# Performance work log

Measured on AMD Instinct MI355X. Metric: run time of the kernel, lower is better.

## Reference

```python
import jax, jax.numpy as jnp
import numpy as np

TEMPERATURE = 0.07
EPS = 1e-07


def setup_inputs() -> dict:
    key = jax.random.key(0)
    kf, kl = jax.random.split(key)
    bsz, n_views, d = 4096, 2, 256
    feats = jax.random.normal(kf, (bsz, n_views, d), dtype=jnp.float32)
    # L2-normalize per view, as in standard SupCon pipelines
    feats = feats / jnp.linalg.norm(feats, axis=-1, keepdims=True)
    labels = jax.random.randint(kl, (bsz,), 0, 3, dtype=jnp.int64 if jax.config.jax_enable_x64 else jnp.int32)
    return {"features": feats, "labels": labels}


def reference(features, labels):
    bsz, n_views, d = features.shape
    n = bsz * n_views
    # torch.cat(torch.unbind(features, dim=1), dim=0): views stacked along batch
    contrast_feature = jnp.transpose(features, (1, 0, 2)).reshape(n, d)
    anchor_feature = contrast_feature  # contrast_mode == 'all'

    # label-equality mask with the module's 1e-7 offset, tiled over views
    mask_small = (labels[:, None] == labels[None, :]).astype(jnp.float32) + EPS
    mask = jnp.tile(mask_small, (n_views, n_views))  # [n, n]

    logits_mask = 1.0 - jnp.eye(n, dtype=jnp.float32)  # zero out self-contrast
    mask_pos = mask * logits_mask
    mask_neg = (1.0 - mask) * logits_mask

    similarity = jnp.exp(jnp.matmul(anchor_feature, contrast_feature.T) / TEMPERATURE)
    pos = jnp.sum(similarity * mask_pos, axis=1)
    neg = jnp.sum(similarity * mask_neg, axis=1)
    loss = -jnp.mean(jnp.log(pos / (pos + neg)))
    return loss
```

## Files before the change

kernel.cpp:

```cpp
#include <hip/hip_runtime.h>
#include <cstdint>

#define BSZ   4096
#define NTOT  8192
#define DIM   256
#define BT    128
#define NCB   (NTOT / BT)
#define NBLK  (NCB * (NCB + 1) / 2)
#define INV_T (1.0f/0.07f)

typedef __bf16 bf16x8 __attribute__((ext_vector_type(8)));
typedef float  f32x4  __attribute__((ext_vector_type(4)));

__device__ __forceinline__ unsigned short f2bf(float f) {
  unsigned int u = __float_as_uint(f);
  u = u + 0x7FFFu + ((u >> 16) & 1u);
  return (unsigned short)(u >> 16);
}


__global__ __launch_bounds__(256) void cvt_kernel(const float* __restrict__ F,
                                                  unsigned short* __restrict__ Xf,
                                                  float* __restrict__ gsum,
                                                  int* __restrict__ gcnt) {
  if (blockIdx.x == 0 && threadIdx.x == 0) { *gsum = 0.f; *gcnt = 0; }
  const int v = blockIdx.x * 256 + threadIdx.x;
  const int T = v >> 9;
  const int c = (v >> 4) & 31;
  const int p = v & 15;
  const int r = T * 16 + p;
  const float* src = F + (size_t)(r & (BSZ - 1)) * (2 * DIM) + (r >> 12) * DIM + c * 8;
  const float4 v0 = *(const float4*)src;
  const float4 v1 = *(const float4*)(src + 4);
  ushort4 o0 = make_ushort4(f2bf(v0.x), f2bf(v0.y), f2bf(v0.z), f2bf(v0.w));
  ushort4 o1 = make_ushort4(f2bf(v1.x), f2bf(v1.y), f2bf(v1.z), f2bf(v1.w));
  *(ushort4*)(Xf + (size_t)v * 8)     = o0;
  *(ushort4*)(Xf + (size_t)v * 8 + 4) = o1;
}

__global__ __launch_bounds__(256, 3) void supcon_kernel(
    const unsigned short* __restrict__ Xf, const int* __restrict__ lab,
    float* __restrict__ partTot, float* __restrict__ partEq) {
  __shared__ float sbuf[1024];

  const int tid  = threadIdx.x;
  const int lane = tid & 63;
  const int wave = tid >> 6;
  const int wr   = (wave >> 1) * 64;
  const int wc   = (wave & 1) * 64;
  const int l15  = lane & 15;
  const int quad = lane >> 4;

  const int b = blockIdx.x;
  const int c = (b & 7) * (NBLK / 8) + (b >> 3);
  int i, j;
  if (c < 1792) {
    const int spo = c >> 6;
    const int w   = c & 63;
    int g1 = 0, rem = spo;
    while (rem >= 7 - g1) { rem -= 7 - g1; ++g1; }
    const int g2 = g1 + 1 + rem;
    i = g1 * 8 + (w >> 3);
    j = g2 * 8 + (w & 7);
  } else {
    const int c2 = c - 1792;
    const int g  = c2 / 36;
    int w = c2 - g * 36;
    int a = 0;
    while (w >= 8 - a) { w -= 8 - a; ++a; }
    i = g * 8 + a;
    j = g * 8 + a + w;
  }
  const int RB = i * BT;
  const int CB = j * BT;

  int colIdx[4], colLab[4];
#pragma unroll
  for (int tc = 0; tc < 4; ++tc) {
    colIdx[tc] = CB + wc + tc * 16 + l15;
    colLab[tc] = lab[colIdx[tc] & (BSZ - 1)];
  }
  int rowLab[4][4];
#pragma unroll
  for (int tr = 0; tr < 4; ++tr)
#pragma unroll
    for (int reg = 0; reg < 4; ++reg)
      rowLab[tr][reg] = lab[(RB + wr + tr * 16 + quad * 4 + reg) & (BSZ - 1)];

  const int TA = (RB >> 4) + (wave >> 1) * 4;
  const int TB = (CB >> 4) + (wave & 1) * 4;
  const int lo = quad * 128 + l15 * 8;

  f32x4 acc[4][4] = {};

#pragma unroll
  for (int kb = 0; kb < 8; ++kb) {
    bf16x8 aF[4], bF[4];
    const int ko = kb * 512 + lo;
#pragma unroll
    for (int t = 0; t < 4; ++t) {
      aF[t] = *(const bf16x8*)(Xf + (size_t)(TA + t) * 4096 + ko);
      bF[t] = *(const bf16x8*)(Xf + (size_t)(TB + t) * 4096 + ko);
    }
#pragma unroll
    for (int tr = 0; tr < 4; ++tr)
#pragma unroll
      for (int tc = 0; tc < 4; ++tc)
        acc[tr][tc] = __builtin_amdgcn_mfma_f32_16x16x32_bf16(
            aF[tr], bF[tc], acc[tr][tc], 0, 0, 0);
  }

  if (i == j) {
#pragma unroll
    for (int tr = 0; tr < 4; ++tr)
#pragma unroll
      for (int tc = 0; tc < 4; ++tc)
#pragma unroll
        for (int reg = 0; reg < 4; ++reg) {
          const int row = RB + wr + tr * 16 + quad * 4 + reg;
          float e = __expf(acc[tr][tc][reg] * INV_T);
          acc[tr][tc][reg] = (colIdx[tc] == row) ? 0.f : e;
        }
  } else {
#pragma unroll
    for (int tr = 0; tr < 4; ++tr)
#pragma unroll
      for (int tc = 0; tc < 4; ++tc)
#pragma unroll
        for (int reg = 0; reg < 4; ++reg)
          acc[tr][tc][reg] = __expf(acc[tr][tc][reg] * INV_T);
  }

#pragma unroll
  for (int tr = 0; tr < 4; ++tr) {
#pragma unroll
    for (int reg = 0; reg < 4; ++reg) {
      float tot = 0.f, eqs = 0.f;
#pragma unroll
      for (int tc = 0; tc < 4; ++tc) {
        const float e = acc[tr][tc][reg];
        tot += e;
        if (colLab[tc] == rowLab[tr][reg]) eqs += e;
      }
#pragma unroll
      for (int off = 1; off < 16; off <<= 1) {
        tot += __shfl_xor(tot, off, 64);
        eqs += __shfl_xor(eqs, off, 64);
      }
      if (l15 == 0) {
        const int rl_ = wr + tr * 16 + quad * 4 + reg;
        sbuf[(wave & 1) * 128 + rl_]       = tot;
        sbuf[256 + (wave & 1) * 128 + rl_] = eqs;
      }
    }
  }
  if (i != j) {
#pragma unroll
    for (int tc = 0; tc < 4; ++tc) {
      float tt = 0.f, te = 0.f;
#pragma unroll
      for (int tr = 0; tr < 4; ++tr)
#pragma unroll
        for (int reg = 0; reg < 4; ++reg) {
          const float e = acc[tr][tc][reg];
          tt += e;
          if (rowLab[tr][reg] == colLab[tc]) te += e;
        }
      tt += __shfl_xor(tt, 16, 64);  te += __shfl_xor(te, 16, 64);
      tt += __shfl_xor(tt, 32, 64);  te += __shfl_xor(te, 32, 64);
      if (quad == 0) {
        const int cl_ = wc + tc * 16 + l15;
        sbuf[512 + (wave >> 1) * 128 + cl_] = tt;
        sbuf[768 + (wave >> 1) * 128 + cl_] = te;
      }
    }
  }
  __syncthreads();

  if (tid < 128) {
    partTot[(size_t)j * NTOT + RB + tid] = sbuf[tid] + sbuf[128 + tid];
    partEq [(size_t)j * NTOT + RB + tid] = sbuf[256 + tid] + sbuf[384 + tid];
  } else if (i != j) {
    const int c2 = tid - 128;
    partTot[(size_t)i * NTOT + CB + c2] = sbuf[512 + c2] + sbuf[640 + c2];
    partEq [(size_t)i * NTOT + CB + c2] = sbuf[768 + c2] + sbuf[896 + c2];
  }
}

__global__ __launch_bounds__(128) void reduce_kernel(
    const float* __restrict__ partTot, const float* __restrict__ partEq,
    float* __restrict__ gsum, int* __restrict__ gcnt,
    unsigned int* __restrict__ out) {
  const int r = blockIdx.x * 128 + threadIdx.x;
  float tot = 0.f, eqs = 0.f;
#pragma unroll 8
  for (int cb = 0; cb < NCB; ++cb) {
    tot += partTot[(size_t)cb * NTOT + r];
    eqs += partEq [(size_t)cb * NTOT + r];
  }
  const float term = __logf((eqs + 1e-7f * tot) / tot);
  __shared__ float red[128];
  red[threadIdx.x] = term;
  __syncthreads();
  for (int step = 64; step > 0; step >>= 1) {
    if (threadIdx.x < step) red[threadIdx.x] += red[threadIdx.x + step];
    __syncthreads();
  }
  if (threadIdx.x == 0) {
    atomicAdd(gsum, red[0]);
    __threadfence();
    const int old = atomicAdd(gcnt, 1);
    if (old == (int)gridDim.x - 1) {
      __threadfence();
      const float total = atomicAdd(gsum, 0.0f);
      const float loss = -total / (float)NTOT;
      const unsigned short bb = f2bf(loss);
      out[0] = ((unsigned int)bb << 16) | (unsigned int)bb;
    }
  }
}

extern "C" void kernel_launch(void* const* d_in, const int* in_sizes, int n_in,
                              void* d_out, int out_size, void* d_ws, size_t ws_size,
                              hipStream_t stream) {
  (void)in_sizes; (void)n_in; (void)out_size; (void)ws_size;
  const float* feats = (const float*)d_in[0];
  const int*   labels = (const int*)d_in[1];

  char* ws = (char*)d_ws;
  unsigned short* Xf = (unsigned short*)ws;
  float* partTot = (float*)(ws + (size_t)NTOT * DIM * 2);
  float* partEq  = partTot + (size_t)NCB * NTOT;
  float* gsum    = partEq  + (size_t)NCB * NTOT;
  int*   gcnt    = (int*)(gsum + 1);

  cvt_kernel<<<NTOT * DIM / 8 / 256, 256, 0, stream>>>(feats, Xf, gsum, gcnt);
  supcon_kernel<<<NBLK, 256, 0, stream>>>(Xf, labels, partTot, partEq);
  reduce_kernel<<<NTOT / 128, 128, 0, stream>>>(partTot, partEq, gsum, gcnt,
                                                (unsigned int*)d_out);
}
```

Measured before the change: 106.8 us.

## Switch similarity GEMM from bf16 to scaled fp8 MFMA

Features are now converted to fp8 (scaled by 4 to use more of the dynamic range) instead of bf16, and the Gram matrix uses fp8 MFMA instructions, with the exponent scale adjusted by 1/16 to undo the scaling. The conversion kernel stages rows through LDS to write the new packed fragment layout. This halves operand bytes and uses the higher-throughput fp8 matrix path, at the cost of much lower precision. Logits are divided by 0.07, so fp8 rounding errors are magnified before the exp, which risks loss accuracy.

```diff
diff --git a/kernel.cpp b/kernel.cpp
--- a/kernel.cpp
+++ b/kernel.cpp
@@ -7,10 +7,9 @@
 #define BT    128
 #define NCB   (NTOT / BT)
 #define NBLK  (NCB * (NCB + 1) / 2)
-#define INV_T (1.0f/0.07f)
-
-typedef __bf16 bf16x8 __attribute__((ext_vector_type(8)));
-typedef float  f32x4  __attribute__((ext_vector_type(4)));
+#define INV_T16 (1.0f/(0.07f*16.0f))
+
+typedef float f32x4 __attribute__((ext_vector_type(4)));
 
 __device__ __forceinline__ unsigned short f2bf(float f) {
   unsigned int u = __float_as_uint(f);
@@ -20,26 +19,41 @@
 
 
 __global__ __launch_bounds__(256) void cvt_kernel(const float* __restrict__ F,
-                                                  unsigned short* __restrict__ Xf,
+                                                  unsigned char* __restrict__ Xf,
                                                   float* __restrict__ gsum,
                                                   int* __restrict__ gcnt) {
+  __shared__ unsigned char lds[32 * 264];
   if (blockIdx.x == 0 && threadIdx.x == 0) { *gsum = 0.f; *gcnt = 0; }
-  const int v = blockIdx.x * 256 + threadIdx.x;
-  const int T = v >> 9;
-  const int c = (v >> 4) & 31;
-  const int p = v & 15;
-  const int r = T * 16 + p;
-  const float* src = F + (size_t)(r & (BSZ - 1)) * (2 * DIM) + (r >> 12) * DIM + c * 8;
-  const float4 v0 = *(const float4*)src;
-  const float4 v1 = *(const float4*)(src + 4);
-  ushort4 o0 = make_ushort4(f2bf(v0.x), f2bf(v0.y), f2bf(v0.z), f2bf(v0.w));
-  ushort4 o1 = make_ushort4(f2bf(v1.x), f2bf(v1.y), f2bf(v1.z), f2bf(v1.w));
-  *(ushort4*)(Xf + (size_t)v * 8)     = o0;
-  *(ushort4*)(Xf + (size_t)v * 8 + 4) = o1;
+  const int t  = threadIdx.x;
+  const int R0 = blockIdx.x * 32;
+#pragma unroll
+  for (int k = 0; k < 8; ++k) {
+    const int f   = t + k * 256;
+    const int row = f >> 6;
+    const int c4  = f & 63;
+    const int r   = R0 + row;
+    const float4 v = *(const float4*)(F + (size_t)(r & (BSZ - 1)) * (2 * DIM)
+                                        + (r >> 12) * DIM + c4 * 4);
+    int w = __builtin_amdgcn_cvt_pk_fp8_f32(v.x * 4.f, v.y * 4.f, 0, false);
+    w     = __builtin_amdgcn_cvt_pk_fp8_f32(v.z * 4.f, v.w * 4.f, w, true);
+    *(int*)(lds + row * 264 + c4 * 4) = w;
+  }
+  __syncthreads();
+#pragma unroll
+  for (int it = 0; it < 2; ++it) {
+    const int o  = t + it * 256;
+    const int Tl = o >> 8, m = (o >> 4) & 15, p = o & 15;
+    const int P  = m >> 2, q = m & 3;
+    const unsigned char* src = lds + (Tl * 16 + p) * 264 + P * 64 + q * 8;
+    const uint2 lo = *(const uint2*)(src);
+    const uint2 hi = *(const uint2*)(src + 32);
+    *(uint4*)(Xf + (size_t)(blockIdx.x * 2 + Tl) * 4096 + m * 256 + p * 16) =
+        make_uint4(lo.x, lo.y, hi.x, hi.y);
+  }
 }
 
 __global__ __launch_bounds__(256, 3) void supcon_kernel(
-    const unsigned short* __restrict__ Xf, const int* __restrict__ lab,
+    const unsigned char* __restrict__ Xf, const int* __restrict__ lab,
     float* __restrict__ partTot, float* __restrict__ partEq) {
   __shared__ float sbuf[1024];
 
@@ -89,25 +103,31 @@
 
   const int TA = (RB >> 4) + (wave >> 1) * 4;
   const int TB = (CB >> 4) + (wave & 1) * 4;
-  const int lo = quad * 128 + l15 * 8;
+  const int lo = quad * 256 + l15 * 16;
 
   f32x4 acc[4][4] = {};
 
 #pragma unroll
-  for (int kb = 0; kb < 8; ++kb) {
-    bf16x8 aF[4], bF[4];
-    const int ko = kb * 512 + lo;
+  for (int P = 0; P < 4; ++P) {
+    ulonglong2 aL[4], bL[4];
+    const int ko = P * 1024 + lo;
 #pragma unroll
     for (int t = 0; t < 4; ++t) {
-      aF[t] = *(const bf16x8*)(Xf + (size_t)(TA + t) * 4096 + ko);
-      bF[t] = *(const bf16x8*)(Xf + (size_t)(TB + t) * 4096 + ko);
-    }
-#pragma unroll
-    for (int tr = 0; tr < 4; ++tr)
-#pragma unroll
-      for (int tc = 0; tc < 4; ++tc)
-        acc[tr][tc] = __builtin_amdgcn_mfma_f32_16x16x32_bf16(
-            aF[tr], bF[tc], acc[tr][tc], 0, 0, 0);
+      aL[t] = *(const ulonglong2*)(Xf + (size_t)(TA + t) * 4096 + ko);
+      bL[t] = *(const ulonglong2*)(Xf + (size_t)(TB + t) * 4096 + ko);
+    }
+#pragma unroll
+    for (int tr = 0; tr < 4; ++tr)
+#pragma unroll
+      for (int tc = 0; tc < 4; ++tc)
+        acc[tr][tc] = __builtin_amdgcn_mfma_f32_16x16x32_fp8_fp8(
+            (long)aL[tr].x, (long)bL[tc].x, acc[tr][tc], 0, 0, 0);
+#pragma unroll
+    for (int tr = 0; tr < 4; ++tr)
+#pragma unroll
+      for (int tc = 0; tc < 4; ++tc)
+        acc[tr][tc] = __builtin_amdgcn_mfma_f32_16x16x32_fp8_fp8(
+            (long)aL[tr].y, (long)bL[tc].y, acc[tr][tc], 0, 0, 0);
   }
 
   if (i == j) {
@@ -118,7 +138,7 @@
 #pragma unroll
         for (int reg = 0; reg < 4; ++reg) {
           const int row = RB + wr + tr * 16 + quad * 4 + reg;
-          float e = __expf(acc[tr][tc][reg] * INV_T);
+          float e = __expf(acc[tr][tc][reg] * INV_T16);
           acc[tr][tc][reg] = (colIdx[tc] == row) ? 0.f : e;
         }
   } else {
@@ -128,7 +148,7 @@
       for (int tc = 0; tc < 4; ++tc)
 #pragma unroll
         for (int reg = 0; reg < 4; ++reg)
-          acc[tr][tc][reg] = __expf(acc[tr][tc][reg] * INV_T);
+          acc[tr][tc][reg] = __expf(acc[tr][tc][reg] * INV_T16);
   }
 
 #pragma unroll
@@ -228,13 +248,13 @@
   const int*   labels = (const int*)d_in[1];
 
   char* ws = (char*)d_ws;
-  unsigned short* Xf = (unsigned short*)ws;
-  float* partTot = (float*)(ws + (size_t)NTOT * DIM * 2);
+  unsigned char* Xf = (unsigned char*)ws;
+  float* partTot = (float*)(ws + (size_t)NTOT * DIM);
   float* partEq  = partTot + (size_t)NCB * NTOT;
   float* gsum    = partEq  + (size_t)NCB * NTOT;
   int*   gcnt    = (int*)(gsum + 1);
 
-  cvt_kernel<<<NTOT * DIM / 8 / 256, 256, 0, stream>>>(feats, Xf, gsum, gcnt);
+  cvt_kernel<<<NTOT / 32, 256, 0, stream>>>(feats, Xf, gsum, gcnt);
   supcon_kernel<<<NBLK, 256, 0, stream>>>(Xf, labels, partTot, partEq);
   reduce_kernel<<<NTOT / 128, 128, 0, stream>>>(partTot, partEq, gsum, gcnt,
                                                 (unsigned int*)d_out);
```

After: 101.2 us. -5.3%, faster.
